# Optimization experiments

Measured on AMD Instinct MI355X. Metric: run time of the kernel, lower is better.

The kernel has to match this reference:

```python
import jax, jax.numpy as jnp
import numpy as np

W = 32            # window_size
HEADS = 8
DH = 64           # dim_head
DIM = 512
NREL = 2 * W - 1  # 63
N = W * W + 1     # 1025 (cls token)
B = 32
EPS = 1e-6
SCALE = DH ** -0.5


def _bias_indices():
    r = np.arange(W)
    gx, gy = np.meshgrid(r, r, indexing='ij')
    grid = np.stack((gx.reshape(-1), gy.reshape(-1)))        # (2, w*w)
    rel = grid[:, :, None] - grid[:, None, :] + (W - 1)       # (2, n, n)
    return (rel[0] * 1 + rel[1] * NREL).astype(np.int32)      # (w*w, w*w)


def setup_inputs() -> dict:
    key = jax.random.key(0)
    ks = jax.random.split(key, 5)
    return {
        'x': jax.random.normal(ks[0], (B, N, DIM), dtype=jnp.float32),
        'w_qkv': jax.random.normal(ks[1], (DIM, 3 * HEADS * DH), dtype=jnp.float32) * 0.02,
        'g': jnp.ones((DH,), dtype=jnp.float32),                      # RMSNorm scale
        'pe_table': jax.random.normal(ks[2], (NREL * NREL, HEADS), dtype=jnp.float32) * 0.02,
        'w_out': jax.random.normal(ks[3], (HEADS * DH, DIM), dtype=jnp.float32) * 0.02,
        'b_out': jnp.zeros((DIM,), dtype=jnp.float32),
        'bias_idx': jnp.asarray(_bias_indices()),
    }


def _rmsnorm(t, g):
    return t * jax.lax.rsqrt(jnp.mean(t * t, axis=-1, keepdims=True) + EPS) * g


def reference(x, w_qkv, g, pe_table, w_out, b_out, bias_idx):
    b, n, _ = x.shape
    # qkv projection; chunk(3) on last dim == leading axis of (3, H, DH)
    qkv = (x @ w_qkv).reshape(b, n, 3, HEADS, DH)
    qkv = jnp.transpose(qkv, (2, 0, 3, 1, 4))                 # (3, b, h, n, d)
    q, k, v = qkv[0], qkv[1], qkv[2]
    dots = jnp.einsum('bhid,bhjd->bhij', _rmsnorm(q, g), _rmsnorm(k, g)) * SCALE
    bias = jnp.transpose(pe_table[bias_idx], (2, 0, 1))       # (h, w*w, w*w)
    dots = dots.at[:, :, 1:, 1:].add(bias)                    # skip cls row/col
    attn = jax.nn.softmax(dots, axis=-1)
    out = jnp.einsum('bhij,bhjd->bhid', attn, v)
    out = jnp.transpose(out, (0, 2, 1, 3)).reshape(b, n, HEADS * DH)
    return out @ w_out + b_out
```

## Files before the change

kernel.cpp:

```cpp
#include <hip/hip_runtime.h>

typedef short bf16x8 __attribute__((ext_vector_type(8)));
typedef float f32x4 __attribute__((ext_vector_type(4)));
typedef float f32x16 __attribute__((ext_vector_type(16)));
typedef unsigned int u32;
typedef u32 u32x4 __attribute__((ext_vector_type(4)));
typedef unsigned short u16;

#define B_    32
#define N_    1025
#define H_    8
#define DIM_  512
#define M_    (B_*N_)
#define QP_   1152
#define BIP_  1152
#define KVSZ_ 67584
#define SCALE_ 0.125f
#define LOG2E_ 1.4426950408889634f
#define COFF_  12.0f

__device__ __forceinline__ u16 f2bf(float f){
  unsigned u = __builtin_bit_cast(unsigned, f);
  u += 0x7FFFu + ((u >> 16) & 1u);
  return (u16)(u >> 16);
}
__device__ __forceinline__ u32 cvtpk(float a, float b){
  u32 r;
  asm("v_cvt_pk_bf16_f32 %0, %1, %2" : "=v"(r) : "v"(a), "v"(b));
  return r;
}
__device__ __forceinline__ void pswap(u32 &a, u32 &b){
  asm("v_permlane32_swap_b32 %0, %1" : "+v"(a), "+v"(b));
}
__device__ __forceinline__ void gll16(const u16* g, u16* l){
  __builtin_amdgcn_global_load_lds((const __attribute__((address_space(1))) u16*)(g),
                                   (__attribute__((address_space(3))) u16*)(l), 16, 0, 0);
}

__global__ __launch_bounds__(256)
void k_conv_x(const float* __restrict__ x, u16* __restrict__ o, int n4){
  int i = blockIdx.x*256 + threadIdx.x;
  if (i >= n4) return;
  float4 v = ((const float4*)x)[i];
  ushort4 r;
  r.x = f2bf(v.x); r.y = f2bf(v.y); r.z = f2bf(v.z); r.w = f2bf(v.w);
  ((ushort4*)o)[i] = r;
}

__global__ __launch_bounds__(256)
void k_transpose(const float* __restrict__ w, u16* __restrict__ wt, int R, int C){
  int i = blockIdx.x*256 + threadIdx.x;
  if (i >= R*C) return;
  int n = i / R, k = i - n*R;
  wt[i] = f2bf(w[k*C + n]);
}

__global__ __launch_bounds__(256)
void k_biasr(const int* __restrict__ idx, const float* __restrict__ pe, u16* __restrict__ br){
  int i_lin = blockIdx.x*256 + threadIdx.x;
  int v = i_lin & 15, hi = (i_lin>>4)&1;
  int t1 = i_lin >> 5;
  int i = t1 % 1152;
  int t2 = t1 / 1152;
  int tj = t2 % 33;
  int h = t2 / 33;
  int j = tj*32 + (v&3) + 8*(v>>2) + 4*hi;
  float val;
  if (j >= 1 && j <= 1024 && i >= 1 && i <= 1024)
    val = pe[idx[(i-1)*1024 + (j-1)]*8 + h] * LOG2E_ - COFF_;
  else
    val = (j <= 1024) ? -COFF_ : -1e9f;
  br[i_lin] = f2bf(val);
}

__global__ __launch_bounds__(256)
void k_ztail(u16* __restrict__ qn, u16* __restrict__ kn2, u16* __restrict__ v2){
  int i = blockIdx.x*256 + threadIdx.x;
  if (i < 2080768){
    int bh = i / (127*64); int r = i - bh*(127*64);
    qn[((size_t)bh*QP_ + 1025 + (r>>6))*64 + (r&63)] = 0;
  } else if (i < 2588672){
    int k = i - 2080768; int bh = k/1984; int r = k - bh*1984;
    int n = 1025 + (r>>6), d = r & 63;
    kn2[(size_t)bh*KVSZ_ + 65536 + ((d>>3)<<8) + ((n&31)<<3) + (d&7)] = 0;
  } else if (i < 3096576){
    int k = i - 2588672; int bh = k/1984; int r = k - bh*1984;
    int n = 1025 + (r>>6), d = r & 63;
    v2[(size_t)bh*KVSZ_ + 65536 + (((n>>3)&3)<<9) + (d<<3) + (n&7)] = 0;
  }
}

__global__ __launch_bounds__(256)
void k_qkv(const u16* __restrict__ xb, const u16* __restrict__ wT, const float* __restrict__ g,
           u16* __restrict__ qn, u16* __restrict__ kn2, u16* __restrict__ v2){
  __shared__ u16 sh[16384];
  const int tid = threadIdx.x;
  const int lane = tid & 63, wid = tid >> 6;
  const int lg = lane >> 4, lr = lane & 15;
  const int wm = wid >> 1, wn = wid & 1;

  int orig = blockIdx.x;
  int xcd = orig & 7, idx = orig >> 3;
  int wgid = (xcd < 4 ? xcd*386 : 1544 + (xcd-4)*385) + idx;
  int mt = wgid / 12, nt = wgid - mt*12;
  const int m0 = mt*128, n0 = nt*128;
  const int qkv_t = nt >> 2;
  const int h = ((nt & 3) << 1) + wn;

  const int srow = tid >> 2;
  const int schunk = (tid & 3) ^ ((tid >> 3) & 3);
  const u16* asrc = xb + (size_t)(m0 + srow)*DIM_ + schunk*8;
  const u16* bsrc = wT + (size_t)(n0 + srow)*DIM_ + schunk*8;
  const int rsw = (lg ^ ((lr>>1)&3)) << 3;

  u16* As = sh;
  u16* Bs = sh + 8192;

  f32x4 acc[4][4];
#pragma unroll
  for (int m=0;m<4;++m)
#pragma unroll
    for (int n=0;n<4;++n) acc[m][n] = {0.f,0.f,0.f,0.f};

  gll16(asrc,            As + wid*512);
  gll16(asrc + 64*DIM_,  As + 2048 + wid*512);
  gll16(bsrc,            Bs + wid*512);
  gll16(bsrc + 64*DIM_,  Bs + 2048 + wid*512);

  for (int s=0; s<16; ++s){
    const int cur = s & 1;
    __syncthreads();
    if (s < 15){
      const int ko = (s+1)*32;
      gll16(asrc + ko,           As + (cur^1)*4096 + wid*512);
      gll16(asrc + ko + 64*DIM_, As + (cur^1)*4096 + 2048 + wid*512);
      gll16(bsrc + ko,           Bs + (cur^1)*4096 + wid*512);
      gll16(bsrc + ko + 64*DIM_, Bs + (cur^1)*4096 + 2048 + wid*512);
    }
    bf16x8 af[4], bf[4];
#pragma unroll
    for (int m=0;m<4;++m) af[m] = *(const bf16x8*)(As + cur*4096 + (64*wm+16*m+lr)*32 + rsw);
#pragma unroll
    for (int n=0;n<4;++n) bf[n] = *(const bf16x8*)(Bs + cur*4096 + (64*wn+16*n+lr)*32 + rsw);
    __builtin_amdgcn_s_setprio(1);
#pragma unroll
    for (int m=0;m<4;++m)
#pragma unroll
      for (int n=0;n<4;++n)
        acc[m][n] = __builtin_amdgcn_mfma_f32_16x16x32_bf16(af[m], bf[n], acc[m][n], 0, 0, 0);
    __builtin_amdgcn_s_setprio(0);
  }

  float gv[4];
#pragma unroll
  for (int n=0;n<4;++n)
    gv[n] = (qkv_t==0) ? g[16*n+lr]*(SCALE_*LOG2E_) : (qkv_t==1 ? g[16*n+lr] : 1.f);

#pragma unroll
  for (int m=0;m<4;++m){
    float rstd[4];
    if (qkv_t < 2){
#pragma unroll
      for (int r=0;r<4;++r){
        float s = 0.f;
#pragma unroll
        for (int n=0;n<4;++n) s += acc[m][n][r]*acc[m][n][r];
        s += __shfl_xor(s, 1); s += __shfl_xor(s, 2);
        s += __shfl_xor(s, 4); s += __shfl_xor(s, 8);
        rstd[r] = rsqrtf(s*(1.f/64.f) + 1e-6f);
      }
    } else {
#pragma unroll
      for (int r=0;r<4;++r) rstd[r] = 1.f;
    }
#pragma unroll
    for (int r=0;r<4;++r){
      int mg = m0 + 64*wm + 16*m + 4*lg + r;
      if (mg < M_){
        int b = mg / N_, pos = mg - b*N_;
        int bh = b*H_ + h;
#pragma unroll
        for (int n=0;n<4;++n){
          int d = 16*n + lr;
          u16 val = f2bf(acc[m][n][r]*rstd[r]*gv[n]);
          if (qkv_t == 0)
            qn[((size_t)bh*QP_ + pos)*64 + d] = val;
          else if (qkv_t == 1)
            kn2[(size_t)bh*KVSZ_ + (pos>>5)*2048 + ((d>>3)<<8) + ((pos&31)<<3) + (d&7)] = val;
          else
            v2[(size_t)bh*KVSZ_ + (pos>>5)*2048 + (((pos>>3)&3)<<9) + (d<<3) + (pos&7)] = val;
        }
      }
    }
  }
}

__global__ __launch_bounds__(256, 4)
void k_attn2(const u16* __restrict__ qn, const u16* __restrict__ kn2, const u16* __restrict__ v2,
             const u16* __restrict__ br, u16* __restrict__ ao){
  __shared__ u16 Ks[2][2048];
  __shared__ u16 Vs[2][2048];
  const int tid = threadIdx.x;
  const int lane = tid & 63, wave = tid >> 6;
  const int il = lane & 31, hi = lane >> 5;
  int wg = ((blockIdx.x & 7) * 288) + (blockIdx.x >> 3);
  int h = wg / 288;
  int rem = wg - h*288;
  int b = rem / 9, qt = rem - (rem/9)*9;
  int bh = b*8 + h;
  int i0 = qt*128 + wave*32;

  const u16* qp = qn + ((size_t)bh*QP_ + (i0 + il))*64 + hi*8;
  bf16x8 qf[4];
#pragma unroll
  for (int c=0;c<4;++c) qf[c] = *(const bf16x8*)(qp + 16*c);

  const u16* ksrc = kn2 + (size_t)bh*KVSZ_ + tid*8;
  const u16* vsrc = v2  + (size_t)bh*KVSZ_ + tid*8;

  gll16(ksrc, &Ks[0][wave*512]);
  gll16(vsrc, &Vs[0][wave*512]);

  f32x16 oA, oB, oS;
#pragma unroll
  for (int r=0;r<16;++r){ oA[r]=0.f; oB[r]=0.f; oS[r]=0.f; }

  const bf16x8 onesf = {0x3F80,0x3F80,0x3F80,0x3F80,0x3F80,0x3F80,0x3F80,0x3F80};

  const u16* bptr = br + (((size_t)(h*33))*BIP_ + (i0 + il))*32 + hi*16;
  bf16x8 bb0 = *(const bf16x8*)(bptr);
  bf16x8 bb1 = *(const bf16x8*)(bptr + 8);

  for (int t=0; t<33; ++t){
    const int cur = t & 1;
    __syncthreads();
    if (t < 32){
      gll16(ksrc + (t+1)*2048, &Ks[cur^1][wave*512]);
      gll16(vsrc + (t+1)*2048, &Vs[cur^1][wave*512]);
    }
    bf16x8 b0 = bb0, b1 = bb1;
    if (t < 32){
      bptr += (size_t)BIP_*32;
      bb0 = *(const bf16x8*)(bptr);
      bb1 = *(const bf16x8*)(bptr + 8);
    }

    f32x16 s;
#pragma unroll
    for (int r=0;r<16;++r) s[r] = 0.f;
    __builtin_amdgcn_s_setprio(1);
#pragma unroll
    for (int c=0;c<4;++c){
      bf16x8 kf = *(const bf16x8*)(&Ks[cur][0] + (2*c + hi)*256 + il*8);
      s = __builtin_amdgcn_mfma_f32_32x32x16_bf16(kf, qf[c], s, 0, 0, 0);
    }
    __builtin_amdgcn_s_setprio(0);

#pragma unroll
    for (int r=0;r<16;++r){
      u16 bv = (r < 8) ? ((u16)b0[r]) : ((u16)b1[r-8]);
      float bf = __builtin_bit_cast(float, ((u32)bv) << 16);
      s[r] = __builtin_amdgcn_exp2f(s[r] + bf);
    }

    u32 X0 = cvtpk(s[0],s[1]),   X1 = cvtpk(s[2],s[3]);
    u32 Y0 = cvtpk(s[4],s[5]),   Y1 = cvtpk(s[6],s[7]);
    u32 X2 = cvtpk(s[8],s[9]),   X3 = cvtpk(s[10],s[11]);
    u32 Y2 = cvtpk(s[12],s[13]), Y3 = cvtpk(s[14],s[15]);
    pswap(X0, Y0); pswap(X1, Y1); pswap(X2, Y2); pswap(X3, Y3);
    u32x4 w0 = {X0, X1, Y0, Y1};
    u32x4 w1 = {X2, X3, Y2, Y3};
    bf16x8 pv0 = __builtin_bit_cast(bf16x8, w0);
    bf16x8 pv1 = __builtin_bit_cast(bf16x8, w1);

    __builtin_amdgcn_s_setprio(1);
#pragma unroll
    for (int c2=0;c2<2;++c2){
      bf16x8 pv = c2 ? pv1 : pv0;
      const u16* vbase = &Vs[cur][0] + (2*c2 + hi)*512;
      bf16x8 vfA = *(const bf16x8*)(vbase + il*8);
      bf16x8 vfB = *(const bf16x8*)(vbase + 256 + il*8);
      oA = __builtin_amdgcn_mfma_f32_32x32x16_bf16(vfA, pv, oA, 0, 0, 0);
      oB = __builtin_amdgcn_mfma_f32_32x32x16_bf16(vfB, pv, oB, 0, 0, 0);
      oS = __builtin_amdgcn_mfma_f32_32x32x16_bf16(onesf, pv, oS, 0, 0, 0);
    }
    __builtin_amdgcn_s_setprio(0);
  }

  int i = i0 + il;
  if (i < N_){
    float inv = 1.f / oS[0];
    u16* op = ao + ((size_t)(b*N_ + i))*DIM_ + h*64;
#pragma unroll
    for (int q=0;q<4;++q)
#pragma unroll
      for (int pr=0;pr<2;++pr){
        int d0 = 8*q + 4*hi + 2*pr;
        u32 wA = cvtpk(oA[4*q+2*pr]*inv, oA[4*q+2*pr+1]*inv);
        u32 wB = cvtpk(oB[4*q+2*pr]*inv, oB[4*q+2*pr+1]*inv);
        *(u32*)(op + d0) = wA;
        *(u32*)(op + 32 + d0) = wB;
      }
  }
}

__global__ __launch_bounds__(256)
void k_oproj(const u16* __restrict__ ab, const u16* __restrict__ wT, const float* __restrict__ bo,
             float* __restrict__ out){
  __shared__ u16 sh[16384];
  const int tid = threadIdx.x;
  const int lane = tid & 63, wid = tid >> 6;
  const int lg = lane >> 4, lr = lane & 15;
  const int wm = wid >> 1, wn = wid & 1;

  int orig = blockIdx.x;
  int xcd = orig & 7, idx = orig >> 3;
  int wgid = (xcd < 4 ? xcd*129 : 516 + (xcd-4)*128) + idx;
  int mt = wgid >> 2, nt = wgid & 3;
  const int m0 = mt*128, n0 = nt*128;

  const int srow = tid >> 2;
  const int schunk = (tid & 3) ^ ((tid >> 3) & 3);
  const u16* asrc = ab + (size_t)(m0 + srow)*DIM_ + schunk*8;
  const u16* bsrc = wT + (size_t)(n0 + srow)*DIM_ + schunk*8;
  const int rsw = (lg ^ ((lr>>1)&3)) << 3;

  u16* As = sh;
  u16* Bs = sh + 8192;

  f32x4 acc[4][4];
#pragma unroll
  for (int m=0;m<4;++m)
#pragma unroll
    for (int n=0;n<4;++n) acc[m][n] = {0.f,0.f,0.f,0.f};

  gll16(asrc,            As + wid*512);
  gll16(asrc + 64*DIM_,  As + 2048 + wid*512);
  gll16(bsrc,            Bs + wid*512);
  gll16(bsrc + 64*DIM_,  Bs + 2048 + wid*512);

  for (int s=0; s<16; ++s){
    const int cur = s & 1;
    __syncthreads();
    if (s < 15){
      const int ko = (s+1)*32;
      gll16(asrc + ko,           As + (cur^1)*4096 + wid*512);
      gll16(asrc + ko + 64*DIM_, As + (cur^1)*4096 + 2048 + wid*512);
      gll16(bsrc + ko,           Bs + (cur^1)*4096 + wid*512);
      gll16(bsrc + ko + 64*DIM_, Bs + (cur^1)*4096 + 2048 + wid*512);
    }
    bf16x8 af[4], bf[4];
#pragma unroll
    for (int m=0;m<4;++m) af[m] = *(const bf16x8*)(As + cur*4096 + (64*wm+16*m+lr)*32 + rsw);
#pragma unroll
    for (int n=0;n<4;++n) bf[n] = *(const bf16x8*)(Bs + cur*4096 + (64*wn+16*n+lr)*32 + rsw);
    __builtin_amdgcn_s_setprio(1);
#pragma unroll
    for (int m=0;m<4;++m)
#pragma unroll
      for (int n=0;n<4;++n)
        acc[m][n] = __builtin_amdgcn_mfma_f32_16x16x32_bf16(af[m], bf[n], acc[m][n], 0, 0, 0);
    __builtin_amdgcn_s_setprio(0);
  }

  float bb[4];
#pragma unroll
  for (int n=0;n<4;++n) bb[n] = bo[n0 + 64*wn + 16*n + lr];
#pragma unroll
  for (int m=0;m<4;++m)
#pragma unroll
    for (int r=0;r<4;++r){
      int mg = m0 + 64*wm + 16*m + 4*lg + r;
      if (mg < M_){
#pragma unroll
        for (int n=0;n<4;++n)
          out[(size_t)mg*DIM_ + n0 + 64*wn + 16*n + lr] = acc[m][n][r] + bb[n];
      }
    }
}

extern "C" void kernel_launch(void* const* d_in, const int* in_sizes, int n_in,
                              void* d_out, int out_size, void* d_ws, size_t ws_size,
                              hipStream_t stream) {
  const float* x     = (const float*)d_in[0];
  const float* w_qkv = (const float*)d_in[1];
  const float* g     = (const float*)d_in[2];
  const float* pe    = (const float*)d_in[3];
  const float* w_out = (const float*)d_in[4];
  const float* b_out = (const float*)d_in[5];
  const int*   bidx  = (const int*)d_in[6];
  float* out = (float*)d_out;

  char* ws = (char*)d_ws;
  u16* xb    = (u16*)(ws);
  u16* wT    = (u16*)(ws + 33587200);
  u16* woT   = (u16*)(ws + 35160064);
  u16* qnb   = (u16*)(ws + 35684352);
  u16* kn2   = (u16*)(ws + 73433088);
  u16* v2    = (u16*)(ws + 108036096);
  u16* biasr = (u16*)(ws + 142639104);
  u16* aob   = xb;

  int n4 = (B_*N_*DIM_)/4;
  k_conv_x<<<(n4+255)/256, 256, 0, stream>>>(x, xb, n4);
  k_transpose<<<(1536*512+255)/256, 256, 0, stream>>>(w_qkv, wT, 512, 1536);
  k_transpose<<<(512*512+255)/256, 256, 0, stream>>>(w_out, woT, 512, 512);
  k_biasr<<<38016, 256, 0, stream>>>(bidx, pe, biasr);
  k_ztail<<<12096, 256, 0, stream>>>(qnb, kn2, v2);

  k_qkv<<<3084, 256, 0, stream>>>(xb, wT, g, qnb, kn2, v2);
  k_attn2<<<2304, 256, 0, stream>>>(qnb, kn2, v2, biasr, aob);
  k_oproj<<<1028, 256, 0, stream>>>(aob, woT, b_out, out);
}
```

Baseline: 300.3 us.

## Process two KV tiles per barrier and fold bias into MFMA accumulator init

The attention loop now stages two 32-key K/V tiles per LDS buffer, so each iteration handles 64 keys and needs half as many barriers and async-load rounds. The KV and bias buffers are padded to 34 tiles, with a final single tile after the loop. The bias is loaded as the initial value of the QK MFMA accumulator, which removes the separate add before exp2. The constant log-offset COFF is dropped from the bias. LDS use doubles and occupancy is lowered to 3 blocks per CU, and dropping the offset could risk exp2 overflow in bf16.

After: 295.7 us. Within noise of the previous version (-1.5%).

```diff
diff --git a/kernel.cpp b/kernel.cpp
--- a/kernel.cpp
+++ b/kernel.cpp
@@ -14,10 +14,11 @@
 #define M_    (B_*N_)
 #define QP_   1152
 #define BIP_  1152
-#define KVSZ_ 67584
+#define NT_   34
+#define KVSZ_ (NT_*2048)
+#define BT_   (BIP_*32)
 #define SCALE_ 0.125f
 #define LOG2E_ 1.4426950408889634f
-#define COFF_  12.0f
 
 __device__ __forceinline__ u16 f2bf(float f){
   unsigned u = __builtin_bit_cast(unsigned, f);
@@ -62,14 +63,14 @@
   int t1 = i_lin >> 5;
   int i = t1 % 1152;
   int t2 = t1 / 1152;
-  int tj = t2 % 33;
-  int h = t2 / 33;
+  int tj = t2 % NT_;
+  int h = t2 / NT_;
   int j = tj*32 + (v&3) + 8*(v>>2) + 4*hi;
   float val;
   if (j >= 1 && j <= 1024 && i >= 1 && i <= 1024)
-    val = pe[idx[(i-1)*1024 + (j-1)]*8 + h] * LOG2E_ - COFF_;
+    val = pe[idx[(i-1)*1024 + (j-1)]*8 + h] * LOG2E_;
   else
-    val = (j <= 1024) ? -COFF_ : -1e9f;
+    val = (j <= 1024) ? 0.f : -1e9f;
   br[i_lin] = f2bf(val);
 }
 
@@ -195,11 +196,50 @@
   }
 }
 
-__global__ __launch_bounds__(256, 4)
+#define TILE(buf, off, B0, B1) do { \
+  f32x16 s; \
+  _Pragma("unroll") \
+  for (int r=0;r<16;++r){ \
+    u16 bv = (r < 8) ? ((u16)(B0)[r]) : ((u16)(B1)[r-8]); \
+    s[r] = __builtin_bit_cast(float, ((u32)bv) << 16); \
+  } \
+  __builtin_amdgcn_s_setprio(1); \
+  _Pragma("unroll") \
+  for (int c=0;c<4;++c){ \
+    bf16x8 kf = *(const bf16x8*)(&Ks[buf][0] + (off) + (2*c + hi)*256 + il*8); \
+    s = __builtin_amdgcn_mfma_f32_32x32x16_bf16(kf, qf[c], s, 0, 0, 0); \
+  } \
+  __builtin_amdgcn_s_setprio(0); \
+  _Pragma("unroll") \
+  for (int r=0;r<16;++r) s[r] = __builtin_amdgcn_exp2f(s[r]); \
+  u32 X0 = cvtpk(s[0],s[1]),   X1 = cvtpk(s[2],s[3]); \
+  u32 Y0 = cvtpk(s[4],s[5]),   Y1 = cvtpk(s[6],s[7]); \
+  u32 X2 = cvtpk(s[8],s[9]),   X3 = cvtpk(s[10],s[11]); \
+  u32 Y2 = cvtpk(s[12],s[13]), Y3 = cvtpk(s[14],s[15]); \
+  pswap(X0, Y0); pswap(X1, Y1); pswap(X2, Y2); pswap(X3, Y3); \
+  u32x4 w0 = {X0, X1, Y0, Y1}; \
+  u32x4 w1 = {X2, X3, Y2, Y3}; \
+  bf16x8 pv0 = __builtin_bit_cast(bf16x8, w0); \
+  bf16x8 pv1 = __builtin_bit_cast(bf16x8, w1); \
+  __builtin_amdgcn_s_setprio(1); \
+  _Pragma("unroll") \
+  for (int c2=0;c2<2;++c2){ \
+    bf16x8 pv = c2 ? pv1 : pv0; \
+    const u16* vb = &Vs[buf][0] + (off) + (2*c2 + hi)*512; \
+    bf16x8 vfA = *(const bf16x8*)(vb + il*8); \
+    bf16x8 vfB = *(const bf16x8*)(vb + 256 + il*8); \
+    oA = __builtin_amdgcn_mfma_f32_32x32x16_bf16(vfA, pv, oA, 0, 0, 0); \
+    oB = __builtin_amdgcn_mfma_f32_32x32x16_bf16(vfB, pv, oB, 0, 0, 0); \
+    oS = __builtin_amdgcn_mfma_f32_32x32x16_bf16(onesf, pv, oS, 0, 0, 0); \
+  } \
+  __builtin_amdgcn_s_setprio(0); \
+} while(0)
+
+__global__ __launch_bounds__(256, 3)
 void k_attn2(const u16* __restrict__ qn, const u16* __restrict__ kn2, const u16* __restrict__ v2,
              const u16* __restrict__ br, u16* __restrict__ ao){
-  __shared__ u16 Ks[2][2048];
-  __shared__ u16 Vs[2][2048];
+  __shared__ u16 Ks[2][4096];
+  __shared__ u16 Vs[2][4096];
   const int tid = threadIdx.x;
   const int lane = tid & 63, wave = tid >> 6;
   const int il = lane & 31, hi = lane >> 5;
@@ -218,8 +258,10 @@
   const u16* ksrc = kn2 + (size_t)bh*KVSZ_ + tid*8;
   const u16* vsrc = v2  + (size_t)bh*KVSZ_ + tid*8;
 
-  gll16(ksrc, &Ks[0][wave*512]);
-  gll16(vsrc, &Vs[0][wave*512]);
+  gll16(ksrc,        &Ks[0][wave*512]);
+  gll16(ksrc + 2048, &Ks[0][2048 + wave*512]);
+  gll16(vsrc,        &Vs[0][wave*512]);
+  gll16(vsrc + 2048, &Vs[0][2048 + wave*512]);
 
   f32x16 oA, oB, oS;
 #pragma unroll
@@ -227,65 +269,32 @@
 
   const bf16x8 onesf = {0x3F80,0x3F80,0x3F80,0x3F80,0x3F80,0x3F80,0x3F80,0x3F80};
 
-  const u16* bptr = br + (((size_t)(h*33))*BIP_ + (i0 + il))*32 + hi*16;
-  bf16x8 bb0 = *(const bf16x8*)(bptr);
-  bf16x8 bb1 = *(const bf16x8*)(bptr + 8);
-
-  for (int t=0; t<33; ++t){
+  const u16* bptr = br + ((size_t)(h*NT_)*BIP_ + (i0 + il))*32 + hi*16;
+  bf16x8 cb0 = *(const bf16x8*)(bptr);
+  bf16x8 cb1 = *(const bf16x8*)(bptr + 8);
+  bf16x8 cb2 = *(const bf16x8*)(bptr + BT_);
+  bf16x8 cb3 = *(const bf16x8*)(bptr + BT_ + 8);
+
+  for (int t=0; t<16; ++t){
     const int cur = t & 1;
     __syncthreads();
-    if (t < 32){
-      gll16(ksrc + (t+1)*2048, &Ks[cur^1][wave*512]);
-      gll16(vsrc + (t+1)*2048, &Vs[cur^1][wave*512]);
-    }
-    bf16x8 b0 = bb0, b1 = bb1;
-    if (t < 32){
-      bptr += (size_t)BIP_*32;
-      bb0 = *(const bf16x8*)(bptr);
-      bb1 = *(const bf16x8*)(bptr + 8);
-    }
-
-    f32x16 s;
-#pragma unroll
-    for (int r=0;r<16;++r) s[r] = 0.f;
-    __builtin_amdgcn_s_setprio(1);
-#pragma unroll
-    for (int c=0;c<4;++c){
-      bf16x8 kf = *(const bf16x8*)(&Ks[cur][0] + (2*c + hi)*256 + il*8);
-      s = __builtin_amdgcn_mfma_f32_32x32x16_bf16(kf, qf[c], s, 0, 0, 0);
-    }
-    __builtin_amdgcn_s_setprio(0);
-
-#pragma unroll
-    for (int r=0;r<16;++r){
-      u16 bv = (r < 8) ? ((u16)b0[r]) : ((u16)b1[r-8]);
-      float bf = __builtin_bit_cast(float, ((u32)bv) << 16);
-      s[r] = __builtin_amdgcn_exp2f(s[r] + bf);
-    }
-
-    u32 X0 = cvtpk(s[0],s[1]),   X1 = cvtpk(s[2],s[3]);
-    u32 Y0 = cvtpk(s[4],s[5]),   Y1 = cvtpk(s[6],s[7]);
-    u32 X2 = cvtpk(s[8],s[9]),   X3 = cvtpk(s[10],s[11]);
-    u32 Y2 = cvtpk(s[12],s[13]), Y3 = cvtpk(s[14],s[15]);
-    pswap(X0, Y0); pswap(X1, Y1); pswap(X2, Y2); pswap(X3, Y3);
-    u32x4 w0 = {X0, X1, Y0, Y1};
-    u32x4 w1 = {X2, X3, Y2, Y3};
-    bf16x8 pv0 = __builtin_bit_cast(bf16x8, w0);
-    bf16x8 pv1 = __builtin_bit_cast(bf16x8, w1);
-
-    __builtin_amdgcn_s_setprio(1);
-#pragma unroll
-    for (int c2=0;c2<2;++c2){
-      bf16x8 pv = c2 ? pv1 : pv0;
-      const u16* vbase = &Vs[cur][0] + (2*c2 + hi)*512;
-      bf16x8 vfA = *(const bf16x8*)(vbase + il*8);
-      bf16x8 vfB = *(const bf16x8*)(vbase + 256 + il*8);
-      oA = __builtin_amdgcn_mfma_f32_32x32x16_bf16(vfA, pv, oA, 0, 0, 0);
-      oB = __builtin_amdgcn_mfma_f32_32x32x16_bf16(vfB, pv, oB, 0, 0, 0);
-      oS = __builtin_amdgcn_mfma_f32_32x32x16_bf16(onesf, pv, oS, 0, 0, 0);
-    }
-    __builtin_amdgcn_s_setprio(0);
-  }
+    {
+      const int base = (2*t+2)*2048;
+      gll16(ksrc + base,        &Ks[cur^1][wave*512]);
+      gll16(ksrc + base + 2048, &Ks[cur^1][2048 + wave*512]);
+      gll16(vsrc + base,        &Vs[cur^1][wave*512]);
+      gll16(vsrc + base + 2048, &Vs[cur^1][2048 + wave*512]);
+    }
+    TILE(cur, 0, cb0, cb1);
+    cb0 = *(const bf16x8*)(bptr + 2*BT_);
+    cb1 = *(const bf16x8*)(bptr + 2*BT_ + 8);
+    TILE(cur, 2048, cb2, cb3);
+    cb2 = *(const bf16x8*)(bptr + 3*BT_);
+    cb3 = *(const bf16x8*)(bptr + 3*BT_ + 8);
+    bptr += 2*BT_;
+  }
+  __syncthreads();
+  TILE(0, 0, cb0, cb1);
 
   int i = i0 + il;
   if (i < N_){
@@ -397,15 +406,15 @@
   u16* woT   = (u16*)(ws + 35160064);
   u16* qnb   = (u16*)(ws + 35684352);
   u16* kn2   = (u16*)(ws + 73433088);
-  u16* v2    = (u16*)(ws + 108036096);
-  u16* biasr = (u16*)(ws + 142639104);
+  u16* v2    = (u16*)(ws + 109084672);
+  u16* biasr = (u16*)(ws + 144736256);
   u16* aob   = xb;
 
   int n4 = (B_*N_*DIM_)/4;
   k_conv_x<<<(n4+255)/256, 256, 0, stream>>>(x, xb, n4);
   k_transpose<<<(1536*512+255)/256, 256, 0, stream>>>(w_qkv, wT, 512, 1536);
   k_transpose<<<(512*512+255)/256, 256, 0, stream>>>(w_out, woT, 512, 512);
-  k_biasr<<<38016, 256, 0, stream>>>(bidx, pe, biasr);
+  k_biasr<<<39168, 256, 0, stream>>>(bidx, pe, biasr);
   k_ztail<<<12096, 256, 0, stream>>>(qnb, kn2, v2);
 
   k_qkv<<<3084, 256, 0, stream>>>(xb, wT, g, qnb, kn2, v2);
```
